# Kernel optimization log

Hardware: AMD Instinct MI355X
Metric: run time of the kernel (lower is better)

## Reference

```python
import jax, jax.numpy as jnp
import numpy as np

N, E, IN, H1, H2, A, B, MAXB = 57344, 458752, 128, 256, 64, 11, 16, 4096
GD = H1  # g_dim = hidden1


def _lin(k, i, o):
    return jax.random.normal(k, (i, o), jnp.float32) / np.sqrt(i).astype(np.float32)


def setup_inputs():
    key = jax.random.key(0)
    ks = jax.random.split(key, 24)
    x = jax.random.normal(ks[0], (N, IN), jnp.float32)
    x = x.at[:, 0].set(1.0)  # every node is a host (x[:,0]==1)
    ei = jax.random.randint(ks[1], (2, E), 0, N, dtype=jnp.int32)
    sizes = [4096] * 12 + [2048] * 4  # sums to N
    batches = jnp.asarray(np.concatenate([[0], np.cumsum(sizes)]), jnp.int32)
    inp = {
        'x': x, 'ei': ei, 'batches': batches, 'max_batch': MAXB,
        'conv1_w': _lin(ks[2], IN, H1), 'conv1_b': jnp.zeros((H1,), jnp.float32),
        'conv2_w': _lin(ks[3], H1, H2), 'conv2_b': jnp.zeros((H2,), jnp.float32),
        # SimpleSelfAttention g0: in=IN, h=H1, g=GD
        'g0_aw': _lin(ks[4], IN, H1), 'g0_ab': jnp.zeros((H1,), jnp.float32),
        'g0_fw': _lin(ks[5], IN, H1), 'g0_fb': jnp.zeros((H1,), jnp.float32),
        'g0_gw': _lin(ks[6], H1 + GD, GD), 'g0_gb': jnp.zeros((GD,), jnp.float32),
        # g1: in=H1, h=H1, g=GD
        'g1_aw': _lin(ks[7], H1, H1), 'g1_ab': jnp.zeros((H1,), jnp.float32),
        'g1_fw': _lin(ks[8], H1, H1), 'g1_fb': jnp.zeros((H1,), jnp.float32),
        'g1_gw': _lin(ks[9], H1 + GD, GD), 'g1_gb': jnp.zeros((GD,), jnp.float32),
        # g2: in=H2, h=H2, g=GD
        'g2_aw': _lin(ks[10], H2, H2), 'g2_ab': jnp.zeros((H2,), jnp.float32),
        'g2_fw': _lin(ks[11], H2, H2), 'g2_fb': jnp.zeros((H2,), jnp.float32),
        'g2_gw': _lin(ks[12], H2 + GD, GD), 'g2_gb': jnp.zeros((GD,), jnp.float32),
        # out MLP head
        'o1_w': _lin(ks[13], H2 + GD, H1), 'o1_b': jnp.zeros((H1,), jnp.float32),
        'o2_w': _lin(ks[14], H1, A), 'o2_b': jnp.zeros((A,), jnp.float32),
    }
    return inp


def reference(x, ei, batches, max_batch,
              conv1_w, conv1_b, conv2_w, conv2_b,
              g0_aw, g0_ab, g0_fw, g0_fb, g0_gw, g0_gb,
              g1_aw, g1_ab, g1_fw, g1_fb, g1_gw, g1_gb,
              g2_aw, g2_ab, g2_fw, g2_fb, g2_gw, g2_gb,
              o1_w, o1_b, o2_w, o2_b):
    n = x.shape[0]
    nb = batches.shape[0] - 1
    idx = jnp.arange(n, dtype=jnp.int32)
    # all nodes are hosts; CSR -> (batch_id, position) for vectorized pad_and_pack
    batch_id = jnp.searchsorted(batches, idx, side='right').astype(jnp.int32) - 1
    pos = idx - batches[batch_id]
    mask = jnp.zeros((nb, max_batch, 1), x.dtype).at[batch_id, pos].set(1.0)

    def pack(h):  # [n, d] -> [nb, max_batch, d] with zero padding
        return jnp.zeros((nb, max_batch, h.shape[-1]), h.dtype).at[batch_id, pos].set(h)

    src_sl = jnp.concatenate([ei[0], idx])  # add self loops
    dst_sl = jnp.concatenate([ei[1], idx])

    def gcn(h, W, b):  # GCNConv: D^{-1/2}(A+I)D^{-1/2} h W + b (deg from target col)
        deg = jax.ops.segment_sum(jnp.ones_like(dst_sl, h.dtype), dst_sl, num_segments=n)
        dis = jnp.where(deg > 0, jax.lax.rsqrt(jnp.maximum(deg, 1.0)), 0.0)
        norm = dis[src_sl] * dis[dst_sl]
        hw = h @ W
        return jax.ops.segment_sum(hw[src_sl] * norm[:, None], dst_sl, num_segments=n) + b

    def attn(v, g, aw, ab, fw, fb, gw, gb):  # SimpleSelfAttention
        att = jax.nn.softmax(v @ aw + ab, axis=-1) * mask
        feat = v @ fw + fb
        o = jnp.sum(att * feat, axis=1)  # [nb, h]
        return g + (jnp.concatenate([o, g], axis=-1) @ gw + gb)

    g = attn(pack(x), jnp.zeros((nb, GD), x.dtype), g0_aw, g0_ab, g0_fw, g0_fb, g0_gw, g0_gb)
    h = jax.nn.relu(gcn(x, conv1_w, conv1_b))
    g = attn(pack(h), g, g1_aw, g1_ab, g1_fw, g1_fb, g1_gw, g1_gb)
    h = jax.nn.relu(gcn(h, conv2_w, conv2_b))
    g = attn(pack(h), g, g2_aw, g2_ab, g2_fw, g2_fb, g2_gw, g2_gb)

    host_z = jnp.concatenate([h, g[batch_id]], axis=1)  # repeat_interleave via gather
    actions = jax.nn.relu(host_z @ o1_w + o1_b) @ o2_w + o2_b  # [n, A]
    out = pack(actions)  # [nb, max_batch, A]
    out = jnp.where(mask > 0, out, -jnp.inf)
    return out.reshape(nb, max_batch * A)  # Categorical logits
```

## Files before the change

### kernel.cpp

```cpp
#include <hip/hip_runtime.h>
#include <math.h>

#define N_NODES 57344
#define N_EDGES 458752
#define DIM_IN 128
#define DIM_H1 256
#define DIM_H2 64
#define DIM_A 11
#define NB 16
#define MAXB 4096
#define OUT_PER_B (MAXB*DIM_A)
#define OUT_SZ (NB*OUT_PER_B)
#define NEG_FILL (-1.0e30f)

typedef unsigned short u16;
typedef unsigned int u32;
typedef __bf16 bf16x8 __attribute__((ext_vector_type(8)));
typedef float f32x4 __attribute__((ext_vector_type(4)));

__device__ __forceinline__ float bflo(u32 u){ union{u32 i; float f;} x; x.i = u<<16; return x.f; }
__device__ __forceinline__ float bfhi(u32 u){ union{u32 i; float f;} x; x.i = u & 0xFFFF0000u; return x.f; }
__device__ __forceinline__ u32 f2bf(float f){ union{float f; u32 i;} x; x.f=f; return (x.i + 0x7FFFu + ((x.i>>16)&1u)) >> 16; }

__device__ __forceinline__ float wave_max(float v){
  #pragma unroll
  for (int off=32; off; off>>=1) v = fmaxf(v, __shfl_xor(v, off));
  return v;
}
__device__ __forceinline__ float wave_sum(float v){
  #pragma unroll
  for (int off=32; off; off>>=1) v += __shfl_xor(v, off);
  return v;
}

__global__ __launch_bounds__(256) void k_init(int* cnt, int* bid, const int* __restrict__ batches,
                                              float* oacc, float* out){
  int i = blockIdx.x*256 + threadIdx.x;
  if (i < N_NODES){
    cnt[i] = 0;
    int lo=0, hi=NB-1;
    while (lo<hi){ int mid=(lo+hi+1)>>1; if (batches[mid]<=i) lo=mid; else hi=mid-1; }
    bid[i]=lo;
  }
  if (i < 3*NB*256) oacc[i] = 0.0f;
  if (i < OUT_SZ) out[i] = NEG_FILL;
}

__global__ __launch_bounds__(256) void k_deg(const int* __restrict__ ei, int* cnt){
  int e = blockIdx.x*256 + threadIdx.x;
  if (e < N_EDGES) atomicAdd(&cnt[ei[N_EDGES + e]], 1);
}

__global__ __launch_bounds__(256) void k_scanA(const int* __restrict__ cnt, int* bsum){
  __shared__ int s[256];
  int t=threadIdx.x; int i=blockIdx.x*256+t;
  s[t]=cnt[i]; __syncthreads();
  for (int off=128; off; off>>=1){ if (t<off) s[t]+=s[t+off]; __syncthreads(); }
  if (t==0) bsum[blockIdx.x]=s[0];
}
__global__ __launch_bounds__(256) void k_scanB(const int* __restrict__ bsum, int* boff){
  __shared__ int s[256];
  int t=threadIdx.x;
  int v = (t < N_NODES/256) ? bsum[t] : 0;
  s[t]=v; __syncthreads();
  for (int o=1;o<256;o<<=1){
    int a = (t>=o) ? s[t-o] : 0;
    __syncthreads();
    s[t] += a;
    __syncthreads();
  }
  if (t < N_NODES/256) boff[t] = s[t] - v;
}
__global__ __launch_bounds__(256) void k_scanC(const int* __restrict__ cnt, const int* __restrict__ boff,
                                               int* rowstart, int* cursor, float* dis){
  __shared__ int s[256];
  int t=threadIdx.x; int i=blockIdx.x*256+t;
  int v=cnt[i]; s[t]=v; __syncthreads();
  for (int off=1; off<256; off<<=1){
    int add = (t>=off)? s[t-off] : 0;
    __syncthreads();
    s[t]+=add;
    __syncthreads();
  }
  int rs = boff[blockIdx.x] + s[t] - v;
  rowstart[i]=rs; cursor[i]=rs;
  dis[i] = rsqrtf(1.0f + (float)v);
}
__global__ __launch_bounds__(256) void k_place(const int* __restrict__ ei, int* cursor, int* csr_src){
  int e = blockIdx.x*256 + threadIdx.x;
  if (e < N_EDGES){
    int s = ei[e], d = ei[N_EDGES+e];
    int slot = atomicAdd(&cursor[d], 1);
    csr_src[slot] = s;
  }
}

__global__ __launch_bounds__(256) void k_cvtx(const float* __restrict__ x, u16* __restrict__ xb){
  int i = blockIdx.x*256 + threadIdx.x;
  float4 v = *(const float4*)(x + (size_t)i*4);
  u32 lo = f2bf(v.x) | (f2bf(v.y)<<16);
  u32 hi = f2bf(v.z) | (f2bf(v.w)<<16);
  *(uint2*)(xb + (size_t)i*4) = make_uint2(lo, hi);
}

__global__ __launch_bounds__(256) void k_prep(
    const float* __restrict__ conv1_w, const float* __restrict__ g0_aw, const float* __restrict__ g0_fw,
    const float* __restrict__ g1_aw, const float* __restrict__ g1_fw, const float* __restrict__ conv2_w,
    const float* __restrict__ g2_aw, const float* __restrict__ g2_fw, const float* __restrict__ o1_w,
    const float* __restrict__ g0_ab, const float* __restrict__ g0_fb,
    const float* __restrict__ g1_ab, const float* __restrict__ g1_fb,
    const float* __restrict__ g2_ab, const float* __restrict__ g2_fb,
    u16* conv1T, u16* Wt0, u16* Wt1, u16* conv2T, u16* Wt2, u16* o1T,
    float* cb0, float* cb1, float* cb2){
  int i = blockIdx.x*256 + threadIdx.x;
  if (i < 32768){ int k=i>>8, n=i&255; conv1T[n*128+k]=(u16)f2bf(conv1_w[i]); return; } i-=32768;
  if (i < 32768){ int k=i>>8, n=i&255; Wt0[n*128+k]=(u16)f2bf(g0_aw[i]); return; } i-=32768;
  if (i < 32768){ int k=i>>8, n=i&255; Wt0[(256+n)*128+k]=(u16)f2bf(g0_fw[i]); return; } i-=32768;
  if (i < 65536){ int k=i>>8, n=i&255; Wt1[n*256+k]=(u16)f2bf(g1_aw[i]); return; } i-=65536;
  if (i < 65536){ int k=i>>8, n=i&255; Wt1[(256+n)*256+k]=(u16)f2bf(g1_fw[i]); return; } i-=65536;
  if (i < 16384){ int k=i>>6, n=i&63;  conv2T[n*256+k]=(u16)f2bf(conv2_w[i]); return; } i-=16384;
  if (i < 4096) { int k=i>>6, n=i&63;  Wt2[n*64+k]=(u16)f2bf(g2_aw[i]); return; } i-=4096;
  if (i < 4096) { int k=i>>6, n=i&63;  Wt2[(64+n)*64+k]=(u16)f2bf(g2_fw[i]); return; } i-=4096;
  if (i < 16384){ int k=i>>8, n=i&255; o1T[n*64+k]=(u16)f2bf(o1_w[i]); return; } i-=16384;
  if (i < 256){ cb0[i]=g0_ab[i]; return; } i-=256;
  if (i < 256){ cb0[256+i]=g0_fb[i]; return; } i-=256;
  if (i < 256){ cb1[i]=g1_ab[i]; return; } i-=256;
  if (i < 256){ cb1[256+i]=g1_fb[i]; return; } i-=256;
  if (i < 64) { cb2[i]=g2_ab[i]; return; } i-=64;
  if (i < 64) { cb2[64+i]=g2_fb[i]; return; }
}

__global__ __launch_bounds__(256) void k_agg1b(const u16* __restrict__ xb, const float* __restrict__ dis,
        const int* __restrict__ rowstart, const int* __restrict__ cnt, const int* __restrict__ csr_src,
        u16* __restrict__ agg){
  int d = (blockIdx.x*256 + threadIdx.x) >> 6;
  int lane = threadIdx.x & 63;
  float dd = dis[d];
  u32 u = *(const u32*)(xb + (size_t)d*DIM_IN + lane*2);
  float ax = bflo(u)*dd*dd, ay = bfhi(u)*dd*dd;
  int base = rowstart[d], c = cnt[d];
  int j = 0;
  for (; j+4 <= c; j += 4){
    int s0=csr_src[base+j+0], s1=csr_src[base+j+1], s2=csr_src[base+j+2], s3=csr_src[base+j+3];
    u32 u0=*(const u32*)(xb+(size_t)s0*DIM_IN+lane*2);
    u32 u1=*(const u32*)(xb+(size_t)s1*DIM_IN+lane*2);
    u32 u2=*(const u32*)(xb+(size_t)s2*DIM_IN+lane*2);
    u32 u3=*(const u32*)(xb+(size_t)s3*DIM_IN+lane*2);
    float n0=dis[s0]*dd, n1=dis[s1]*dd, n2=dis[s2]*dd, n3=dis[s3]*dd;
    ax=fmaf(bflo(u0),n0,ax); ay=fmaf(bfhi(u0),n0,ay);
    ax=fmaf(bflo(u1),n1,ax); ay=fmaf(bfhi(u1),n1,ay);
    ax=fmaf(bflo(u2),n2,ax); ay=fmaf(bfhi(u2),n2,ay);
    ax=fmaf(bflo(u3),n3,ax); ay=fmaf(bfhi(u3),n3,ay);
  }
  for (; j<c; ++j){
    int s = csr_src[base+j];
    float nrm = dis[s]*dd;
    u32 us = *(const u32*)(xb + (size_t)s*DIM_IN + lane*2);
    ax = fmaf(bflo(us), nrm, ax);
    ay = fmaf(bfhi(us), nrm, ay);
  }
  *(u32*)(agg + (size_t)d*DIM_IN + lane*2) = f2bf(ax) | (f2bf(ay)<<16);
}

__global__ __launch_bounds__(256) void k_agg2b(const u16* __restrict__ hw, const float* __restrict__ dis,
        const int* __restrict__ rowstart, const int* __restrict__ cnt, const int* __restrict__ csr_src,
        const float* __restrict__ b2, u16* __restrict__ h2){
  int d = (blockIdx.x*256 + threadIdx.x) >> 6;
  int lane = threadIdx.x & 63;
  float dd = dis[d];
  float acc = bflo((u32)hw[(size_t)d*DIM_H2 + lane]) * dd*dd;
  int base = rowstart[d], c = cnt[d];
  int j = 0;
  for (; j+4 <= c; j += 4){
    int s0=csr_src[base+j+0], s1=csr_src[base+j+1], s2=csr_src[base+j+2], s3=csr_src[base+j+3];
    u16 v0=hw[(size_t)s0*DIM_H2+lane], v1=hw[(size_t)s1*DIM_H2+lane];
    u16 v2=hw[(size_t)s2*DIM_H2+lane], v3=hw[(size_t)s3*DIM_H2+lane];
    float n0=dis[s0]*dd, n1=dis[s1]*dd, n2=dis[s2]*dd, n3=dis[s3]*dd;
    acc=fmaf(bflo((u32)v0),n0,acc); acc=fmaf(bflo((u32)v1),n1,acc);
    acc=fmaf(bflo((u32)v2),n2,acc); acc=fmaf(bflo((u32)v3),n3,acc);
  }
  for (; j<c; ++j){
    int s = csr_src[base+j];
    acc = fmaf(bflo((u32)hw[(size_t)s*DIM_H2 + lane]), dis[s]*dd, acc);
  }
  h2[(size_t)d*DIM_H2 + lane] = (u16)f2bf(fmaxf(acc + b2[lane], 0.0f));
}

__global__ __launch_bounds__(256) void k_mm(const u16* __restrict__ A, const u16* __restrict__ Wt,
        const float* __restrict__ bias, const float* __restrict__ rowbias, const int* __restrict__ bid,
        u16* __restrict__ C, int K, int Ncol, int flags){
  __shared__ u16 As[128][40];
  __shared__ u16 Bs[64][40];
  const int t = threadIdx.x;
  const int row0 = blockIdx.x*128, col0 = blockIdx.y*64;
  const int lane = t & 63, w = t >> 6;
  const int lr = lane & 15, q = lane >> 4;
  f32x4 acc[2][4];
  #pragma unroll
  for (int r=0;r<2;++r){
    #pragma unroll
    for (int c=0;c<4;++c){ f32x4 z = {}; acc[r][c] = z; }
  }
  for (int k0=0; k0<K; k0+=32){
    #pragma unroll
    for (int i=0;i<2;++i){
      int ch = t + i*256;
      int r = ch>>2, ko = (ch&3)*8;
      *(uint4*)(&As[r][ko]) = *(const uint4*)(A + (size_t)(row0+r)*K + k0 + ko);
    }
    {
      int r = t>>2, ko = (t&3)*8;
      *(uint4*)(&Bs[r][ko]) = *(const uint4*)(Wt + (size_t)(col0+r)*K + k0 + ko);
    }
    __syncthreads();
    bf16x8 af0 = *(const bf16x8*)(&As[w*32 + lr][q*8]);
    bf16x8 af1 = *(const bf16x8*)(&As[w*32 + 16 + lr][q*8]);
    #pragma unroll
    for (int c=0;c<4;++c){
      bf16x8 bfr = *(const bf16x8*)(&Bs[c*16 + lr][q*8]);
      acc[0][c] = __builtin_amdgcn_mfma_f32_16x16x32_bf16(af0, bfr, acc[0][c], 0,0,0);
      acc[1][c] = __builtin_amdgcn_mfma_f32_16x16x32_bf16(af1, bfr, acc[1][c], 0,0,0);
    }
    __syncthreads();
  }
  float bcol[4];
  #pragma unroll
  for (int c=0;c<4;++c){
    int col = col0 + c*16 + lr;
    float bv = 0.f;
    if (flags & 4) bv += bias[col];
    if (flags & 2) bv += rowbias[(size_t)bid[row0]*Ncol + col];
    bcol[c] = bv;
  }
  #pragma unroll
  for (int r=0;r<2;++r){
    #pragma unroll
    for (int c=0;c<4;++c){
      int col = col0 + c*16 + lr;
      #pragma unroll
      for (int i=0;i<4;++i){
        int row = row0 + w*32 + r*16 + q*4 + i;
        float v = acc[r][c][i] + bcol[c];
        if (flags & 1) v = fmaxf(v, 0.f);
        C[(size_t)row*Ncol + col] = (u16)f2bf(v);
      }
    }
  }
}

template<int DIN>
__global__ __launch_bounds__(256,2) void k_attn3(const u16* __restrict__ V, const u16* __restrict__ Wt,
        const float* __restrict__ cb, const int* __restrict__ bid, float* __restrict__ o){
  constexpr int KS = DIN/32;
  __shared__ u16 As[128][40];
  __shared__ u16 Bs[64][40];
  const int t = threadIdx.x;
  const int node0 = blockIdx.x*128;
  const int lane = t & 63, w = t >> 6;
  const int lr = lane & 15, q = lane >> 4;
  f32x4 sacc[4][2][4];
  #pragma unroll
  for (int cc=0;cc<4;++cc)
    #pragma unroll
    for (int rf=0;rf<2;++rf)
      #pragma unroll
      for (int cf=0;cf<4;++cf){ f32x4 z = {}; sacc[cc][rf][cf] = z; }
  #pragma unroll
  for (int cc=0;cc<4;++cc){
    for (int k0=0;k0<KS;++k0){
      #pragma unroll
      for (int i=0;i<2;++i){
        int ch = t + i*256;
        int r = ch>>2, ko = (ch&3)*8;
        *(uint4*)(&As[r][ko]) = *(const uint4*)(V + (size_t)(node0+r)*DIN + k0*32 + ko);
      }
      {
        int r = t>>2, ko = (t&3)*8;
        *(uint4*)(&Bs[r][ko]) = *(const uint4*)(Wt + (size_t)(cc*64+r)*DIN + k0*32 + ko);
      }
      __syncthreads();
      bf16x8 a0 = *(const bf16x8*)(&As[w*32 + lr][q*8]);
      bf16x8 a1 = *(const bf16x8*)(&As[w*32 + 16 + lr][q*8]);
      #pragma unroll
      for (int cf=0;cf<4;++cf){
        bf16x8 b = *(const bf16x8*)(&Bs[cf*16 + lr][q*8]);
        sacc[cc][0][cf] = __builtin_amdgcn_mfma_f32_16x16x32_bf16(a0, b, sacc[cc][0][cf], 0,0,0);
        sacc[cc][1][cf] = __builtin_amdgcn_mfma_f32_16x16x32_bf16(a1, b, sacc[cc][1][cf], 0,0,0);
      }
      __syncthreads();
    }
  }
  #pragma unroll
  for (int cc=0;cc<4;++cc)
    #pragma unroll
    for (int cf=0;cf<4;++cf){
      float bv = cb[cc*64 + cf*16 + lr];
      #pragma unroll
      for (int rf=0;rf<2;++rf)
        #pragma unroll
        for (int i=0;i<4;++i) sacc[cc][rf][cf][i] += bv;
    }
  float m[2][4], iz[2][4];
  #pragma unroll
  for (int rf=0;rf<2;++rf){
    #pragma unroll
    for (int i=0;i<4;++i){
      float mx = -1e30f;
      #pragma unroll
      for (int cc=0;cc<4;++cc)
        #pragma unroll
        for (int cf=0;cf<4;++cf) mx = fmaxf(mx, sacc[cc][rf][cf][i]);
      #pragma unroll
      for (int off=1; off<16; off<<=1) mx = fmaxf(mx, __shfl_xor(mx, off));
      float zz = 0.f;
      #pragma unroll
      for (int cc=0;cc<4;++cc)
        #pragma unroll
        for (int cf=0;cf<4;++cf) zz += __expf(sacc[cc][rf][cf][i] - mx);
      #pragma unroll
      for (int off=1; off<16; off<<=1) zz += __shfl_xor(zz, off);
      m[rf][i] = mx; iz[rf][i] = 1.0f/zz;
    }
  }
  const int bb = bid[node0];
  #pragma unroll
  for (int cc=0;cc<4;++cc){
    f32x4 facc[2][4];
    #pragma unroll
    for (int rf=0;rf<2;++rf)
      #pragma unroll
      for (int cf=0;cf<4;++cf){ f32x4 z = {}; facc[rf][cf] = z; }
    for (int k0=0;k0<KS;++k0){
      #pragma unroll
      for (int i=0;i<2;++i){
        int ch = t + i*256;
        int r = ch>>2, ko = (ch&3)*8;
        *(uint4*)(&As[r][ko]) = *(const uint4*)(V + (size_t)(node0+r)*DIN + k0*32 + ko);
      }
      {
        int r = t>>2, ko = (t&3)*8;
        *(uint4*)(&Bs[r][ko]) = *(const uint4*)(Wt + (size_t)(256+cc*64+r)*DIN + k0*32 + ko);
      }
      __syncthreads();
      bf16x8 a0 = *(const bf16x8*)(&As[w*32 + lr][q*8]);
      bf16x8 a1 = *(const bf16x8*)(&As[w*32 + 16 + lr][q*8]);
      #pragma unroll
      for (int cf=0;cf<4;++cf){
        bf16x8 b = *(const bf16x8*)(&Bs[cf*16 + lr][q*8]);
        facc[0][cf] = __builtin_amdgcn_mfma_f32_16x16x32_bf16(a0, b, facc[0][cf], 0,0,0);
        facc[1][cf] = __builtin_amdgcn_mfma_f32_16x16x32_bf16(a1, b, facc[1][cf], 0,0,0);
      }
      __syncthreads();
    }
    #pragma unroll
    for (int cf=0;cf<4;++cf){
      float fb = cb[256 + cc*64 + cf*16 + lr];
      float cs = 0.f;
      #pragma unroll
      for (int rf=0;rf<2;++rf)
        #pragma unroll
        for (int i=0;i<4;++i){
          float p = __expf(sacc[cc][rf][cf][i] - m[rf][i]) * iz[rf][i];
          cs = fmaf(p, facc[rf][cf][i] + fb, cs);
        }
      cs += __shfl_xor(cs, 16);
      cs += __shfl_xor(cs, 32);
      if (q == 0) atomicAdd(&o[bb*256 + cc*64 + cf*16 + lr], cs);
    }
  }
}

template<int DIN, int H>
__global__ __launch_bounds__(256) void k_attnf(const u16* __restrict__ V, const u16* __restrict__ Wt,
        const float* __restrict__ cb, const int* __restrict__ bid, float* __restrict__ o){
  constexpr int CF  = H/64;
  constexpr int KS  = DIN/32;
  constexpr int AST = DIN + 8;
  constexpr int SST = H + 4;
  __shared__ u16 As[32*AST];
  __shared__ u16 Ssh[32*SST];
  __shared__ u16 Fsh[32*SST];
  __shared__ float mZ[2][32];
  const int t = threadIdx.x;
  const int node0 = blockIdx.x*32;
  const int lane = t & 63, w = t >> 6;
  const int lr = lane & 15, q = lane >> 4;
  #pragma unroll
  for (int i = 0; i < (32*DIN/8)/256; ++i){
    int ch = t + i*256;
    int r = ch / (DIN/8), co = (ch % (DIN/8))*8;
    *(uint4*)(&As[r*AST + co]) = *(const uint4*)(V + (size_t)(node0+r)*DIN + co);
  }
  __syncthreads();
  #pragma unroll
  for (int ph = 0; ph < 2; ++ph){
    f32x4 acc[2][CF];
    #pragma unroll
    for (int r=0;r<2;++r){
      #pragma unroll
      for (int c=0;c<CF;++c){ f32x4 z = {}; acc[r][c] = z; }
    }
    #pragma unroll
    for (int k=0;k<KS;++k){
      bf16x8 a0 = *(const bf16x8*)(&As[lr*AST + k*32 + q*8]);
      bf16x8 a1 = *(const bf16x8*)(&As[(16+lr)*AST + k*32 + q*8]);
      #pragma unroll
      for (int c=0;c<CF;++c){
        int col = ph*H + w*(16*CF) + c*16 + lr;
        bf16x8 b = *(const bf16x8*)(Wt + (size_t)col*DIN + k*32 + q*8);
        acc[0][c] = __builtin_amdgcn_mfma_f32_16x16x32_bf16(a0, b, acc[0][c], 0,0,0);
        acc[1][c] = __builtin_amdgcn_mfma_f32_16x16x32_bf16(a1, b, acc[1][c], 0,0,0);
      }
    }
    u16* dst = ph ? Fsh : Ssh;
    #pragma unroll
    for (int c=0;c<CF;++c){
      int colL = w*(16*CF) + c*16 + lr;
      float bias = cb[ph*H + colL];
      #pragma unroll
      for (int rf=0; rf<2; ++rf){
        #pragma unroll
        for (int i=0;i<4;++i){
          int row = rf*16 + q*4 + i;
          dst[row*SST + colL] = (u16)f2bf(acc[rf][c][i] + bias);
        }
      }
    }
    if (ph==0){
      __syncthreads();
      #pragma unroll
      for (int nn=0; nn<8; ++nn){
        int n = w*8 + nn;
        constexpr int VPL = H/64;
        float vals[VPL]; float mx = -1e30f;
        if constexpr (VPL == 4){
          uint2 uv = *(const uint2*)(&Ssh[n*SST + lane*4]);
          vals[0]=bflo(uv.x); vals[1]=bfhi(uv.x); vals[2]=bflo(uv.y); vals[3]=bfhi(uv.y);
          mx = fmaxf(fmaxf(vals[0],vals[1]), fmaxf(vals[2],vals[3]));
        } else {
          vals[0] = bflo((u32)Ssh[n*SST + lane]);
          mx = vals[0];
        }
        mx = wave_max(mx);
        float z = 0.f;
        #pragma unroll
        for (int i=0;i<VPL;++i) z += __expf(vals[i]-mx);
        z = wave_sum(z);
        if (lane==0){ mZ[0][n]=mx; mZ[1][n]=1.0f/z; }
      }
    }
  }
  __syncthreads();
  const int col = t % H;
  constexpr int NPER = 32*H/256;
  const int n0 = (t / H) * NPER;
  float acc2 = 0.f;
  #pragma unroll 8
  for (int n=n0; n<n0+NPER; ++n){
    float s = bflo((u32)Ssh[n*SST + col]);
    float f = bflo((u32)Fsh[n*SST + col]);
    acc2 = fmaf(__expf(s - mZ[0][n]) * mZ[1][n], f, acc2);
  }
  atomicAdd(&o[bid[node0]*H + col], acc2);
}

template<int H, bool HASG>
__global__ __launch_bounds__(256) void k_gup2(const float* __restrict__ o, const float* __restrict__ gprev,
        const float* __restrict__ gw, const float* __restrict__ gb, float* __restrict__ gout){
  constexpr int KT = H + (HASG ? 256 : 0);
  constexpr int KPS = KT/8;
  __shared__ float vsh[KT];
  __shared__ float red[8][33];
  const int b = blockIdx.x;
  const int c = threadIdx.x & 31;
  const int s = threadIdx.x >> 5;
  const int col = blockIdx.y*32 + c;
  for (int k=threadIdx.x; k<KT; k+=256)
    vsh[k] = (k < H) ? o[b*H + k] : gprev[b*256 + (k - H)];
  __syncthreads();
  float acc = 0.f;
  const float* wp = gw + (size_t)(s*KPS)*256 + col;
  #pragma unroll 8
  for (int i=0;i<KPS;++i)
    acc = fmaf(vsh[s*KPS+i], wp[(size_t)i*256], acc);
  red[s][c] = acc;
  __syncthreads();
  if (s==0){
    float sum = 0.f;
    #pragma unroll
    for (int j=0;j<8;++j) sum += red[j][c];
    float gp = HASG ? gprev[b*256+col] : 0.f;
    gout[b*256+col] = gp + sum + gb[col];
  }
}

__global__ __launch_bounds__(256) void k_hb2(const float* __restrict__ g2, const float* __restrict__ o1w,
                                             const float* __restrict__ o1b, float* __restrict__ hb){
  __shared__ float vsh[256];
  __shared__ float red[8][33];
  const int b = blockIdx.x;
  const int c = threadIdx.x & 31;
  const int s = threadIdx.x >> 5;
  const int col = blockIdx.y*32 + c;
  vsh[threadIdx.x] = g2[b*256 + threadIdx.x];
  __syncthreads();
  float acc = 0.f;
  const float* wp = o1w + (size_t)(64 + s*32)*256 + col;
  #pragma unroll 8
  for (int i=0;i<32;++i)
    acc = fmaf(vsh[s*32+i], wp[(size_t)i*256], acc);
  red[s][c] = acc;
  __syncthreads();
  if (s==0){
    float sum = 0.f;
    #pragma unroll
    for (int j=0;j<8;++j) sum += red[j][c];
    hb[b*256+col] = sum + o1b[col];
  }
}

__global__ __launch_bounds__(256) void k_head2(const u16* __restrict__ z, const float* __restrict__ w,
        const float* __restrict__ bvec, const int* __restrict__ bid, const int* __restrict__ batches,
        float* __restrict__ out){
  __shared__ float zs[16][257];
  int t = threadIdx.x;
  int g0 = blockIdx.x*16;
  #pragma unroll
  for (int i=0;i<2;++i){
    int ch = t + i*256;
    int v = ch>>5, ko=(ch&31)*8;
    uint4 qv = *(const uint4*)(z + (size_t)(g0+v)*256 + ko);
    zs[v][ko+0]=bflo(qv.x); zs[v][ko+1]=bfhi(qv.x);
    zs[v][ko+2]=bflo(qv.y); zs[v][ko+3]=bfhi(qv.y);
    zs[v][ko+4]=bflo(qv.z); zs[v][ko+5]=bfhi(qv.z);
    zs[v][ko+6]=bflo(qv.w); zs[v][ko+7]=bfhi(qv.w);
  }
  __syncthreads();
  int v = t >> 4, c = t & 15;
  if (c < DIM_A){
    float acc = bvec[c];
    for (int k=0;k<256;++k) acc = fmaf(zs[v][k], w[k*DIM_A + c], acc);
    int node = g0 + v;
    int bb = bid[node];
    out[(size_t)bb*OUT_PER_B + (size_t)(node - batches[bb])*DIM_A + c] = acc;
  }
}

extern "C" void kernel_launch(void* const* d_in, const int* in_sizes, int n_in,
                              void* d_out, int out_size, void* d_ws, size_t ws_size,
                              hipStream_t stream){
  const float* x       = (const float*)d_in[0];
  const int*   ei      = (const int*)d_in[1];
  const int*   batches = (const int*)d_in[2];
  const float* conv1_w = (const float*)d_in[4];
  const float* conv1_b = (const float*)d_in[5];
  const float* conv2_w = (const float*)d_in[6];
  const float* conv2_b = (const float*)d_in[7];
  const float* g0_aw = (const float*)d_in[8];  const float* g0_ab = (const float*)d_in[9];
  const float* g0_fw = (const float*)d_in[10]; const float* g0_fb = (const float*)d_in[11];
  const float* g0_gw = (const float*)d_in[12]; const float* g0_gb = (const float*)d_in[13];
  const float* g1_aw = (const float*)d_in[14]; const float* g1_ab = (const float*)d_in[15];
  const float* g1_fw = (const float*)d_in[16]; const float* g1_fb = (const float*)d_in[17];
  const float* g1_gw = (const float*)d_in[18]; const float* g1_gb = (const float*)d_in[19];
  const float* g2_aw = (const float*)d_in[20]; const float* g2_ab = (const float*)d_in[21];
  const float* g2_fw = (const float*)d_in[22]; const float* g2_fb = (const float*)d_in[23];
  const float* g2_gw = (const float*)d_in[24]; const float* g2_gb = (const float*)d_in[25];
  const float* o1_w  = (const float*)d_in[26]; const float* o1_b  = (const float*)d_in[27];
  const float* o2_w  = (const float*)d_in[28]; const float* o2_b  = (const float*)d_in[29];
  float* out = (float*)d_out;

  char* W = (char*)d_ws;
  size_t off = 0;
  auto alloc = [&](size_t bytes)->void*{
    off = (off + 255) & ~(size_t)255;
    void* p = W + off; off += bytes; return p;
  };
  float* dis      = (float*)alloc(N_NODES*4);
  int*   cnt      = (int*)  alloc(N_NODES*4);
  int*   bid      = (int*)  alloc(N_NODES*4);
  int*   rowstart = (int*)  alloc(N_NODES*4);
  int*   cursor   = (int*)  alloc(N_NODES*4);
  int*   csr_src  = (int*)  alloc(N_EDGES*4);
  int*   bsum     = (int*)  alloc(256*4);
  int*   boff     = (int*)  alloc(256*4);
  float* o0       = (float*)alloc(NB*256*4);
  float* o1a      = (float*)alloc(NB*256*4);
  float* o2a      = (float*)alloc(NB*256*4);
  float* gv0      = (float*)alloc(NB*256*4);
  float* gv1      = (float*)alloc(NB*256*4);
  float* gv2      = (float*)alloc(NB*256*4);
  float* hb       = (float*)alloc(NB*256*4);
  float* cb0      = (float*)alloc(512*4);
  float* cb1      = (float*)alloc(512*4);
  float* cb2      = (float*)alloc(128*4);
  u16* conv1T = (u16*)alloc(32768*2);
  u16* Wt0    = (u16*)alloc(65536*2);
  u16* Wt1    = (u16*)alloc(131072*2);
  u16* conv2T = (u16*)alloc(16384*2);
  u16* Wt2    = (u16*)alloc(8192*2);
  u16* o1T    = (u16*)alloc(16384*2);
  u16* h1b    = (u16*)alloc((size_t)N_NODES*DIM_H1*2);
  u16* X      = (u16*)alloc((size_t)N_NODES*DIM_IN*2);
  u16* agg1b  = (u16*)alloc((size_t)N_NODES*DIM_IN*2);
  u16* xb    = X;
  u16* hw2b  = X;
  u16* h2b   = X + (size_t)N_NODES*DIM_H2;
  u16* z     = h1b;

  k_init <<<OUT_SZ/256, 256, 0, stream>>>(cnt, bid, batches, o0, out);
  k_deg  <<<N_EDGES/256, 256, 0, stream>>>(ei, cnt);
  k_scanA<<<N_NODES/256, 256, 0, stream>>>(cnt, bsum);
  k_scanB<<<1, 256, 0, stream>>>(bsum, boff);
  k_scanC<<<N_NODES/256, 256, 0, stream>>>(cnt, boff, rowstart, cursor, dis);
  k_place<<<N_EDGES/256, 256, 0, stream>>>(ei, cursor, csr_src);

  k_cvtx <<<N_NODES*DIM_IN/4/256, 256, 0, stream>>>(x, xb);
  k_prep <<<(270336+1152+255)/256, 256, 0, stream>>>(conv1_w, g0_aw, g0_fw, g1_aw, g1_fw, conv2_w,
            g2_aw, g2_fw, o1_w, g0_ab, g0_fb, g1_ab, g1_fb, g2_ab, g2_fb,
            conv1T, Wt0, Wt1, conv2T, Wt2, o1T, cb0, cb1, cb2);

  k_agg1b<<<N_NODES/4, 256, 0, stream>>>(xb, dis, rowstart, cnt, csr_src, agg1b);
  k_mm   <<<dim3(N_NODES/128, 4), 256, 0, stream>>>(agg1b, conv1T, conv1_b, nullptr, nullptr,
                                                    h1b, DIM_IN, DIM_H1, 4|1);
  k_attn3<128><<<N_NODES/128, 256, 0, stream>>>(xb, Wt0, cb0, bid, o0);
  k_gup2<256,false><<<dim3(NB,8), 256, 0, stream>>>(o0, nullptr, g0_gw, g0_gb, gv0);

  k_attn3<256><<<N_NODES/128, 256, 0, stream>>>(h1b, Wt1, cb1, bid, o1a);
  k_gup2<256,true><<<dim3(NB,8), 256, 0, stream>>>(o1a, gv0, g1_gw, g1_gb, gv1);

  k_mm   <<<dim3(N_NODES/128, 1), 256, 0, stream>>>(h1b, conv2T, nullptr, nullptr, nullptr,
                                                    hw2b, DIM_H1, DIM_H2, 0);
  k_agg2b<<<N_NODES/4, 256, 0, stream>>>(hw2b, dis, rowstart, cnt, csr_src, conv2_b, h2b);

  k_attnf<64,64><<<N_NODES/32, 256, 0, stream>>>(h2b, Wt2, cb2, bid, o2a);
  k_gup2<64,true><<<dim3(NB,8), 256, 0, stream>>>(o2a, gv1, g2_gw, g2_gb, gv2);

  k_hb2  <<<dim3(NB,8), 256, 0, stream>>>(gv2, o1_w, o1_b, hb);
  k_mm   <<<dim3(N_NODES/128, 4), 256, 0, stream>>>(h2b, o1T, nullptr, hb, bid, z, DIM_H2, 256, 2|1);
  k_head2<<<N_NODES/16, 256, 0, stream>>>(z, o2_w, o2_b, bid, batches, out);

  (void)in_sizes; (void)n_in; (void)out_size; (void)ws_size;
}
```

Measured before the change: 440.2 us.

## Keep attention node tile resident in LDS and double-buffer weight tiles

The attention kernel now loads its 128-node input tile into shared memory once, instead of re-reading it from global memory for every output chunk and every K step in both the score and feature passes. Weight tiles are double-buffered, so each step needs one barrier instead of two and the next weight load overlaps the current MFMA work. The score and feature passes become one flattened step loop. For DIN=256 the larger LDS footprint (about 66KB plus B buffers) may limit the two blocks per CU the launch bounds ask for.

```diff
diff --git a/kernel.cpp b/kernel.cpp
--- a/kernel.cpp
+++ b/kernel.cpp
@@ -249,15 +249,28 @@
 }
 
 template<int DIN>
-__global__ __launch_bounds__(256,2) void k_attn3(const u16* __restrict__ V, const u16* __restrict__ Wt,
+__global__ __launch_bounds__(256,2) void k_attn4(const u16* __restrict__ V, const u16* __restrict__ Wt,
         const float* __restrict__ cb, const int* __restrict__ bid, float* __restrict__ o){
-  constexpr int KS = DIN/32;
-  __shared__ u16 As[128][40];
-  __shared__ u16 Bs[64][40];
+  constexpr int KS  = DIN/32;
+  constexpr int NJ  = 8*KS;
+  constexpr int AST = DIN + 8;
+  __shared__ u16 As[128*AST];
+  __shared__ u16 Bs[2][64][40];
   const int t = threadIdx.x;
   const int node0 = blockIdx.x*128;
   const int lane = t & 63, w = t >> 6;
   const int lr = lane & 15, q = lane >> 4;
+  #pragma unroll
+  for (int i = 0; i < 128*DIN/(8*256); ++i){
+    int ch = t + i*256;
+    int r = ch / (DIN/8), co = (ch % (DIN/8))*8;
+    *(uint4*)(&As[r*AST + co]) = *(const uint4*)(V + (size_t)(node0+r)*DIN + co);
+  }
+  auto stageB = [&](int j, int buf){
+    int chunk = j / KS, k0 = j % KS;
+    int r = t>>2, ko = (t&3)*8;
+    *(uint4*)(&Bs[buf][r][ko]) = *(const uint4*)(Wt + (size_t)(chunk*64 + r)*DIN + k0*32 + ko);
+  };
   f32x4 sacc[4][2][4];
   #pragma unroll
   for (int cc=0;cc<4;++cc)
@@ -265,30 +278,21 @@
     for (int rf=0;rf<2;++rf)
       #pragma unroll
       for (int cf=0;cf<4;++cf){ f32x4 z = {}; sacc[cc][rf][cf] = z; }
-  #pragma unroll
-  for (int cc=0;cc<4;++cc){
-    for (int k0=0;k0<KS;++k0){
-      #pragma unroll
-      for (int i=0;i<2;++i){
-        int ch = t + i*256;
-        int r = ch>>2, ko = (ch&3)*8;
-        *(uint4*)(&As[r][ko]) = *(const uint4*)(V + (size_t)(node0+r)*DIN + k0*32 + ko);
-      }
-      {
-        int r = t>>2, ko = (t&3)*8;
-        *(uint4*)(&Bs[r][ko]) = *(const uint4*)(Wt + (size_t)(cc*64+r)*DIN + k0*32 + ko);
-      }
-      __syncthreads();
-      bf16x8 a0 = *(const bf16x8*)(&As[w*32 + lr][q*8]);
-      bf16x8 a1 = *(const bf16x8*)(&As[w*32 + 16 + lr][q*8]);
-      #pragma unroll
-      for (int cf=0;cf<4;++cf){
-        bf16x8 b = *(const bf16x8*)(&Bs[cf*16 + lr][q*8]);
-        sacc[cc][0][cf] = __builtin_amdgcn_mfma_f32_16x16x32_bf16(a0, b, sacc[cc][0][cf], 0,0,0);
-        sacc[cc][1][cf] = __builtin_amdgcn_mfma_f32_16x16x32_bf16(a1, b, sacc[cc][1][cf], 0,0,0);
-      }
-      __syncthreads();
-    }
+  stageB(0, 0);
+  __syncthreads();
+  #pragma unroll
+  for (int j=0; j<4*KS; ++j){
+    if (j+1 < NJ) stageB(j+1, (j+1)&1);
+    const int k0 = j % KS, chunk = j / KS, buf = j & 1;
+    bf16x8 a0 = *(const bf16x8*)(&As[(w*32 + lr)*AST + k0*32 + q*8]);
+    bf16x8 a1 = *(const bf16x8*)(&As[(w*32 + 16 + lr)*AST + k0*32 + q*8]);
+    #pragma unroll
+    for (int cf=0;cf<4;++cf){
+      bf16x8 b = *(const bf16x8*)(&Bs[buf][cf*16 + lr][q*8]);
+      sacc[chunk][0][cf] = __builtin_amdgcn_mfma_f32_16x16x32_bf16(a0, b, sacc[chunk][0][cf], 0,0,0);
+      sacc[chunk][1][cf] = __builtin_amdgcn_mfma_f32_16x16x32_bf16(a1, b, sacc[chunk][1][cf], 0,0,0);
+    }
+    __syncthreads();
   }
   #pragma unroll
   for (int cc=0;cc<4;++cc)
@@ -323,50 +327,46 @@
     }
   }
   const int bb = bid[node0];
-  #pragma unroll
-  for (int cc=0;cc<4;++cc){
-    f32x4 facc[2][4];
-    #pragma unroll
-    for (int rf=0;rf<2;++rf)
-      #pragma unroll
-      for (int cf=0;cf<4;++cf){ f32x4 z = {}; facc[rf][cf] = z; }
-    for (int k0=0;k0<KS;++k0){
-      #pragma unroll
-      for (int i=0;i<2;++i){
-        int ch = t + i*256;
-        int r = ch>>2, ko = (ch&3)*8;
-        *(uint4*)(&As[r][ko]) = *(const uint4*)(V + (size_t)(node0+r)*DIN + k0*32 + ko);
+  f32x4 facc[2][4];
+  #pragma unroll
+  for (int rf=0;rf<2;++rf)
+    #pragma unroll
+    for (int cf=0;cf<4;++cf){ f32x4 z = {}; facc[rf][cf] = z; }
+  #pragma unroll
+  for (int j=4*KS; j<NJ; ++j){
+    if (j+1 < NJ) stageB(j+1, (j+1)&1);
+    const int k0 = j % KS, chunk = j / KS, buf = j & 1;
+    bf16x8 a0 = *(const bf16x8*)(&As[(w*32 + lr)*AST + k0*32 + q*8]);
+    bf16x8 a1 = *(const bf16x8*)(&As[(w*32 + 16 + lr)*AST + k0*32 + q*8]);
+    #pragma unroll
+    for (int cf=0;cf<4;++cf){
+      bf16x8 b = *(const bf16x8*)(&Bs[buf][cf*16 + lr][q*8]);
+      facc[0][cf] = __builtin_amdgcn_mfma_f32_16x16x32_bf16(a0, b, facc[0][cf], 0,0,0);
+      facc[1][cf] = __builtin_amdgcn_mfma_f32_16x16x32_bf16(a1, b, facc[1][cf], 0,0,0);
+    }
+    if (k0 == KS-1){
+      const int sc = chunk - 4;
+      #pragma unroll
+      for (int cf=0;cf<4;++cf){
+        float fb = cb[chunk*64 + cf*16 + lr];
+        float cs = 0.f;
+        #pragma unroll
+        for (int rf=0;rf<2;++rf)
+          #pragma unroll
+          for (int i=0;i<4;++i){
+            float p = __expf(sacc[sc][rf][cf][i] - m[rf][i]) * iz[rf][i];
+            cs = fmaf(p, facc[rf][cf][i] + fb, cs);
+          }
+        cs += __shfl_xor(cs, 16);
+        cs += __shfl_xor(cs, 32);
+        if (q == 0) atomicAdd(&o[bb*256 + sc*64 + cf*16 + lr], cs);
       }
-      {
-        int r = t>>2, ko = (t&3)*8;
-        *(uint4*)(&Bs[r][ko]) = *(const uint4*)(Wt + (size_t)(256+cc*64+r)*DIN + k0*32 + ko);
-      }
-      __syncthreads();
-      bf16x8 a0 = *(const bf16x8*)(&As[w*32 + lr][q*8]);
-      bf16x8 a1 = *(const bf16x8*)(&As[w*32 + 16 + lr][q*8]);
-      #pragma unroll
-      for (int cf=0;cf<4;++cf){
-        bf16x8 b = *(const bf16x8*)(&Bs[cf*16 + lr][q*8]);
-        facc[0][cf] = __builtin_amdgcn_mfma_f32_16x16x32_bf16(a0, b, facc[0][cf], 0,0,0);
-        facc[1][cf] = __builtin_amdgcn_mfma_f32_16x16x32_bf16(a1, b, facc[1][cf], 0,0,0);
-      }
-      __syncthreads();
-    }
-    #pragma unroll
-    for (int cf=0;cf<4;++cf){
-      float fb = cb[256 + cc*64 + cf*16 + lr];
-      float cs = 0.f;
       #pragma unroll
       for (int rf=0;rf<2;++rf)
         #pragma unroll
-        for (int i=0;i<4;++i){
-          float p = __expf(sacc[cc][rf][cf][i] - m[rf][i]) * iz[rf][i];
-          cs = fmaf(p, facc[rf][cf][i] + fb, cs);
-        }
-      cs += __shfl_xor(cs, 16);
-      cs += __shfl_xor(cs, 32);
-      if (q == 0) atomicAdd(&o[bb*256 + cc*64 + cf*16 + lr], cs);
-    }
+        for (int cf=0;cf<4;++cf){ f32x4 z = {}; facc[rf][cf] = z; }
+    }
+    __syncthreads();
   }
 }
 
@@ -622,10 +622,10 @@
   k_agg1b<<<N_NODES/4, 256, 0, stream>>>(xb, dis, rowstart, cnt, csr_src, agg1b);
   k_mm   <<<dim3(N_NODES/128, 4), 256, 0, stream>>>(agg1b, conv1T, conv1_b, nullptr, nullptr,
                                                     h1b, DIM_IN, DIM_H1, 4|1);
-  k_attn3<128><<<N_NODES/128, 256, 0, stream>>>(xb, Wt0, cb0, bid, o0);
+  k_attn4<128><<<N_NODES/128, 256, 0, stream>>>(xb, Wt0, cb0, bid, o0);
   k_gup2<256,false><<<dim3(NB,8), 256, 0, stream>>>(o0, nullptr, g0_gw, g0_gb, gv0);
 
-  k_attn3<256><<<N_NODES/128, 256, 0, stream>>>(h1b, Wt1, cb1, bid, o1a);
+  k_attn4<256><<<N_NODES/128, 256, 0, stream>>>(h1b, Wt1, cb1, bid, o1a);
   k_gup2<256,true><<<dim3(NB,8), 256, 0, stream>>>(o1a, gv0, g1_gw, g1_gb, gv1);
 
   k_mm   <<<dim3(N_NODES/128, 1), 256, 0, stream>>>(h1b, conv2T, nullptr, nullptr, nullptr,
```

Measured after the change: 423.3 us. 1.04x faster.

## Split fused attention kernel into score-softmax and feature-reduce kernels via bf16 P buffer

Applied to the files above, without the earlier changes.

Replaces the single attention kernel, which held all 256 score columns in registers for 128 rows, with two kernels over 64-row tiles. The first computes scores and softmax, reducing max and sum across waves through shared memory, and writes the probabilities to a global bf16 buffer. The second computes the feature GEMM, reads the probabilities back and does the weighted column sum with atomics. This lowers register pressure so occupancy can go from 2 to 4 blocks per CU. The cost is an extra round trip of about 29 MB through global memory per layer and bf16 rounding of the probabilities.

```diff
diff --git a/kernel.cpp b/kernel.cpp
--- a/kernel.cpp
+++ b/kernel.cpp
@@ -249,124 +249,148 @@
 }
 
 template<int DIN>
-__global__ __launch_bounds__(256,2) void k_attn3(const u16* __restrict__ V, const u16* __restrict__ Wt,
-        const float* __restrict__ cb, const int* __restrict__ bid, float* __restrict__ o){
+__global__ __launch_bounds__(256,4) void k_attnS(const u16* __restrict__ V, const u16* __restrict__ Wt,
+        const float* __restrict__ cb, u16* __restrict__ P){
   constexpr int KS = DIN/32;
-  __shared__ u16 As[128][40];
-  __shared__ u16 Bs[64][40];
+  __shared__ u16 As[64][40];
+  __shared__ u16 Bs[256][40];
+  __shared__ float mred[4][64];
+  __shared__ float zred[4][64];
   const int t = threadIdx.x;
-  const int node0 = blockIdx.x*128;
+  const int node0 = blockIdx.x*64;
   const int lane = t & 63, w = t >> 6;
   const int lr = lane & 15, q = lane >> 4;
-  f32x4 sacc[4][2][4];
-  #pragma unroll
-  for (int cc=0;cc<4;++cc)
-    #pragma unroll
-    for (int rf=0;rf<2;++rf)
-      #pragma unroll
-      for (int cf=0;cf<4;++cf){ f32x4 z = {}; sacc[cc][rf][cf] = z; }
-  #pragma unroll
-  for (int cc=0;cc<4;++cc){
-    for (int k0=0;k0<KS;++k0){
-      #pragma unroll
-      for (int i=0;i<2;++i){
-        int ch = t + i*256;
-        int r = ch>>2, ko = (ch&3)*8;
-        *(uint4*)(&As[r][ko]) = *(const uint4*)(V + (size_t)(node0+r)*DIN + k0*32 + ko);
+  f32x4 sacc[4][4];
+  #pragma unroll
+  for (int rf=0;rf<4;++rf)
+    #pragma unroll
+    for (int cf=0;cf<4;++cf){ f32x4 z = {}; sacc[rf][cf] = z; }
+  for (int k0=0;k0<KS;++k0){
+    { int r=t>>2, ko=(t&3)*8;
+      *(uint4*)(&As[r][ko]) = *(const uint4*)(V + (size_t)(node0+r)*DIN + k0*32 + ko); }
+    #pragma unroll
+    for (int i=0;i<4;++i){
+      int ch = t + i*256; int c = ch>>2, ko=(ch&3)*8;
+      *(uint4*)(&Bs[c][ko]) = *(const uint4*)(Wt + (size_t)c*DIN + k0*32 + ko);
+    }
+    __syncthreads();
+    bf16x8 a[4];
+    #pragma unroll
+    for (int rf=0;rf<4;++rf) a[rf] = *(const bf16x8*)(&As[rf*16+lr][q*8]);
+    #pragma unroll
+    for (int cf=0;cf<4;++cf){
+      bf16x8 b = *(const bf16x8*)(&Bs[w*64+cf*16+lr][q*8]);
+      #pragma unroll
+      for (int rf=0;rf<4;++rf)
+        sacc[rf][cf] = __builtin_amdgcn_mfma_f32_16x16x32_bf16(a[rf], b, sacc[rf][cf], 0,0,0);
+    }
+    __syncthreads();
+  }
+  #pragma unroll
+  for (int cf=0;cf<4;++cf){
+    float bv = cb[w*64 + cf*16 + lr];
+    #pragma unroll
+    for (int rf=0;rf<4;++rf)
+      #pragma unroll
+      for (int i=0;i<4;++i) sacc[rf][cf][i] += bv;
+  }
+  #pragma unroll
+  for (int rf=0;rf<4;++rf)
+    #pragma unroll
+    for (int i=0;i<4;++i){
+      float pm = sacc[rf][0][i];
+      #pragma unroll
+      for (int cf=1;cf<4;++cf) pm = fmaxf(pm, sacc[rf][cf][i]);
+      #pragma unroll
+      for (int off=1; off<16; off<<=1) pm = fmaxf(pm, __shfl_xor(pm, off));
+      if (lr==0) mred[w][rf*16 + q*4 + i] = pm;
+    }
+  __syncthreads();
+  float m[4][4];
+  #pragma unroll
+  for (int rf=0;rf<4;++rf)
+    #pragma unroll
+    for (int i=0;i<4;++i){
+      int row = rf*16 + q*4 + i;
+      m[rf][i] = fmaxf(fmaxf(mred[0][row],mred[1][row]), fmaxf(mred[2][row],mred[3][row]));
+    }
+  #pragma unroll
+  for (int rf=0;rf<4;++rf)
+    #pragma unroll
+    for (int i=0;i<4;++i){
+      float pz = 0.f;
+      #pragma unroll
+      for (int cf=0;cf<4;++cf) pz += __expf(sacc[rf][cf][i] - m[rf][i]);
+      #pragma unroll
+      for (int off=1; off<16; off<<=1) pz += __shfl_xor(pz, off);
+      if (lr==0) zred[w][rf*16 + q*4 + i] = pz;
+    }
+  __syncthreads();
+  #pragma unroll
+  for (int rf=0;rf<4;++rf)
+    #pragma unroll
+    for (int i=0;i<4;++i){
+      int row = rf*16 + q*4 + i;
+      float iz = 1.0f/(zred[0][row]+zred[1][row]+zred[2][row]+zred[3][row]);
+      #pragma unroll
+      for (int cf=0;cf<4;++cf)
+        P[(size_t)(node0+row)*256 + w*64 + cf*16 + lr] = (u16)f2bf(__expf(sacc[rf][cf][i]-m[rf][i])*iz);
+    }
+}
+
+template<int DIN>
+__global__ __launch_bounds__(256,4) void k_attnF(const u16* __restrict__ V, const u16* __restrict__ Wt,
+        const float* __restrict__ cb, const u16* __restrict__ P, const int* __restrict__ bid,
+        float* __restrict__ o){
+  constexpr int KS = DIN/32;
+  __shared__ u16 As[64][40];
+  __shared__ u16 Bs[256][40];
+  const int t = threadIdx.x;
+  const int node0 = blockIdx.x*64;
+  const int lane = t & 63, w = t >> 6;
+  const int lr = lane & 15, q = lane >> 4;
+  f32x4 facc[4][4];
+  #pragma unroll
+  for (int rf=0;rf<4;++rf)
+    #pragma unroll
+    for (int cf=0;cf<4;++cf){ f32x4 z = {}; facc[rf][cf] = z; }
+  for (int k0=0;k0<KS;++k0){
+    { int r=t>>2, ko=(t&3)*8;
+      *(uint4*)(&As[r][ko]) = *(const uint4*)(V + (size_t)(node0+r)*DIN + k0*32 + ko); }
+    #pragma unroll
+    for (int i=0;i<4;++i){
+      int ch = t + i*256; int c = ch>>2, ko=(ch&3)*8;
+      *(uint4*)(&Bs[c][ko]) = *(const uint4*)(Wt + (size_t)(256+c)*DIN + k0*32 + ko);
+    }
+    __syncthreads();
+    bf16x8 a[4];
+    #pragma unroll
+    for (int rf=0;rf<4;++rf) a[rf] = *(const bf16x8*)(&As[rf*16+lr][q*8]);
+    #pragma unroll
+    for (int cf=0;cf<4;++cf){
+      bf16x8 b = *(const bf16x8*)(&Bs[w*64+cf*16+lr][q*8]);
+      #pragma unroll
+      for (int rf=0;rf<4;++rf)
+        facc[rf][cf] = __builtin_amdgcn_mfma_f32_16x16x32_bf16(a[rf], b, facc[rf][cf], 0,0,0);
+    }
+    __syncthreads();
+  }
+  const int bb = bid[node0];
+  #pragma unroll
+  for (int cf=0;cf<4;++cf){
+    const int col = w*64 + cf*16 + lr;
+    float fb = cb[256 + col];
+    float cs = 0.f;
+    #pragma unroll
+    for (int rf=0;rf<4;++rf)
+      #pragma unroll
+      for (int i=0;i<4;++i){
+        float p = bflo((u32)P[(size_t)(node0 + rf*16 + q*4 + i)*256 + col]);
+        cs = fmaf(p, facc[rf][cf][i] + fb, cs);
       }
-      {
-        int r = t>>2, ko = (t&3)*8;
-        *(uint4*)(&Bs[r][ko]) = *(const uint4*)(Wt + (size_t)(cc*64+r)*DIN + k0*32 + ko);
-      }
-      __syncthreads();
-      bf16x8 a0 = *(const bf16x8*)(&As[w*32 + lr][q*8]);
-      bf16x8 a1 = *(const bf16x8*)(&As[w*32 + 16 + lr][q*8]);
-      #pragma unroll
-      for (int cf=0;cf<4;++cf){
-        bf16x8 b = *(const bf16x8*)(&Bs[cf*16 + lr][q*8]);
-        sacc[cc][0][cf] = __builtin_amdgcn_mfma_f32_16x16x32_bf16(a0, b, sacc[cc][0][cf], 0,0,0);
-        sacc[cc][1][cf] = __builtin_amdgcn_mfma_f32_16x16x32_bf16(a1, b, sacc[cc][1][cf], 0,0,0);
-      }
-      __syncthreads();
-    }
-  }
-  #pragma unroll
-  for (int cc=0;cc<4;++cc)
-    #pragma unroll
-    for (int cf=0;cf<4;++cf){
-      float bv = cb[cc*64 + cf*16 + lr];
-      #pragma unroll
-      for (int rf=0;rf<2;++rf)
-        #pragma unroll
-        for (int i=0;i<4;++i) sacc[cc][rf][cf][i] += bv;
-    }
-  float m[2][4], iz[2][4];
-  #pragma unroll
-  for (int rf=0;rf<2;++rf){
-    #pragma unroll
-    for (int i=0;i<4;++i){
-      float mx = -1e30f;
-      #pragma unroll
-      for (int cc=0;cc<4;++cc)
-        #pragma unroll
-        for (int cf=0;cf<4;++cf) mx = fmaxf(mx, sacc[cc][rf][cf][i]);
-      #pragma unroll
-      for (int off=1; off<16; off<<=1) mx = fmaxf(mx, __shfl_xor(mx, off));
-      float zz = 0.f;
-      #pragma unroll
-      for (int cc=0;cc<4;++cc)
-        #pragma unroll
-        for (int cf=0;cf<4;++cf) zz += __expf(sacc[cc][rf][cf][i] - mx);
-      #pragma unroll
-      for (int off=1; off<16; off<<=1) zz += __shfl_xor(zz, off);
-      m[rf][i] = mx; iz[rf][i] = 1.0f/zz;
-    }
-  }
-  const int bb = bid[node0];
-  #pragma unroll
-  for (int cc=0;cc<4;++cc){
-    f32x4 facc[2][4];
-    #pragma unroll
-    for (int rf=0;rf<2;++rf)
-      #pragma unroll
-      for (int cf=0;cf<4;++cf){ f32x4 z = {}; facc[rf][cf] = z; }
-    for (int k0=0;k0<KS;++k0){
-      #pragma unroll
-      for (int i=0;i<2;++i){
-        int ch = t + i*256;
-        int r = ch>>2, ko = (ch&3)*8;
-        *(uint4*)(&As[r][ko]) = *(const uint4*)(V + (size_t)(node0+r)*DIN + k0*32 + ko);
-      }
-      {
-        int r = t>>2, ko = (t&3)*8;
-        *(uint4*)(&Bs[r][ko]) = *(const uint4*)(Wt + (size_t)(256+cc*64+r)*DIN + k0*32 + ko);
-      }
-      __syncthreads();
-      bf16x8 a0 = *(const bf16x8*)(&As[w*32 + lr][q*8]);
-      bf16x8 a1 = *(const bf16x8*)(&As[w*32 + 16 + lr][q*8]);
-      #pragma unroll
-      for (int cf=0;cf<4;++cf){
-        bf16x8 b = *(const bf16x8*)(&Bs[cf*16 + lr][q*8]);
-        facc[0][cf] = __builtin_amdgcn_mfma_f32_16x16x32_bf16(a0, b, facc[0][cf], 0,0,0);
-        facc[1][cf] = __builtin_amdgcn_mfma_f32_16x16x32_bf16(a1, b, facc[1][cf], 0,0,0);
-      }
-      __syncthreads();
-    }
-    #pragma unroll
-    for (int cf=0;cf<4;++cf){
-      float fb = cb[256 + cc*64 + cf*16 + lr];
-      float cs = 0.f;
-      #pragma unroll
-      for (int rf=0;rf<2;++rf)
-        #pragma unroll
-        for (int i=0;i<4;++i){
-          float p = __expf(sacc[cc][rf][cf][i] - m[rf][i]) * iz[rf][i];
-          cs = fmaf(p, facc[rf][cf][i] + fb, cs);
-        }
-      cs += __shfl_xor(cs, 16);
-      cs += __shfl_xor(cs, 32);
-      if (q == 0) atomicAdd(&o[bb*256 + cc*64 + cf*16 + lr], cs);
-    }
+    cs += __shfl_xor(cs, 16);
+    cs += __shfl_xor(cs, 32);
+    if (q == 0) atomicAdd(&o[bb*256 + col], cs);
   }
 }
 
@@ -602,6 +626,7 @@
   u16* h1b    = (u16*)alloc((size_t)N_NODES*DIM_H1*2);
   u16* X      = (u16*)alloc((size_t)N_NODES*DIM_IN*2);
   u16* agg1b  = (u16*)alloc((size_t)N_NODES*DIM_IN*2);
+  u16* P      = (u16*)alloc((size_t)N_NODES*256*2);
   u16* xb    = X;
   u16* hw2b  = X;
   u16* h2b   = X + (size_t)N_NODES*DIM_H2;
@@ -622,10 +647,12 @@
   k_agg1b<<<N_NODES/4, 256, 0, stream>>>(xb, dis, rowstart, cnt, csr_src, agg1b);
   k_mm   <<<dim3(N_NODES/128, 4), 256, 0, stream>>>(agg1b, conv1T, conv1_b, nullptr, nullptr,
                                                     h1b, DIM_IN, DIM_H1, 4|1);
-  k_attn3<128><<<N_NODES/128, 256, 0, stream>>>(xb, Wt0, cb0, bid, o0);
+  k_attnS<128><<<N_NODES/64, 256, 0, stream>>>(xb, Wt0, cb0, P);
+  k_attnF<128><<<N_NODES/64, 256, 0, stream>>>(xb, Wt0, cb0, P, bid, o0);
   k_gup2<256,false><<<dim3(NB,8), 256, 0, stream>>>(o0, nullptr, g0_gw, g0_gb, gv0);
 
-  k_attn3<256><<<N_NODES/128, 256, 0, stream>>>(h1b, Wt1, cb1, bid, o1a);
+  k_attnS<256><<<N_NODES/64, 256, 0, stream>>>(h1b, Wt1, cb1, P);
+  k_attnF<256><<<N_NODES/64, 256, 0, stream>>>(h1b, Wt1, cb1, P, bid, o1a);
   k_gup2<256,true><<<dim3(NB,8), 256, 0, stream>>>(o1a, gv0, g1_gw, g1_gb, gv1);
 
   k_mm   <<<dim3(N_NODES/128, 1), 256, 0, stream>>>(h1b, conv2T, nullptr, nullptr, nullptr,
```

New measurement: 453.9 us. 3.1% more time.
